# Performance work log

Measured on AMD Instinct MI355X. Metric: run time of the kernel, lower is better.

Reference implementation:

```python
import jax, jax.numpy as jnp
import numpy as np

N, D, H, F = 50000, 128, 8, 512
HD = D // H
EPS_BN = 1e-5


def _batchnorm(x, gamma, beta):
    # BatchNorm1d in training mode: per-feature batch stats over node dim
    m = x.mean(axis=0)
    v = x.var(axis=0)
    return (x - m) * jax.lax.rsqrt(v + EPS_BN) * gamma + beta


def setup_inputs() -> dict:
    key = jax.random.key(0)
    ks = jax.random.split(key, 12)
    s = 0.05
    return {
        "src": jax.random.normal(ks[0], (N, D), jnp.float32),
        "edge_index": jax.random.randint(ks[1], (2, 800000), 0, N, jnp.int64),
        "q_w": jax.random.normal(ks[2], (D, D), jnp.float32) * s,
        "q_b": jnp.zeros((D,), jnp.float32),
        "k_w": jax.random.normal(ks[3], (D, D), jnp.float32) * s,
        "v_w": jax.random.normal(ks[4], (D, D), jnp.float32) * s,
        "out_w": jax.random.normal(ks[5], (D, D), jnp.float32) * s,
        "out_b": jnp.zeros((D,), jnp.float32),
        "g1": jnp.ones((D,), jnp.float32),
        "b1": jnp.zeros((D,), jnp.float32),
        "lin1_w": jax.random.normal(ks[6], (F, D), jnp.float32) * s,
        "lin1_b": jnp.zeros((F,), jnp.float32),
        "lin2_w": jax.random.normal(ks[7], (D, F), jnp.float32) * s,
        "lin2_b": jnp.zeros((D,), jnp.float32),
        "g2": jnp.ones((D,), jnp.float32),
        "b2": jnp.zeros((D,), jnp.float32),
    }


def reference(src, edge_index, q_w, q_b, k_w, v_w, out_w, out_b,
              g1, b1, lin1_w, lin1_b, lin2_w, lin2_b, g2, b2):
    n = src.shape[0]
    # add self loops, then attention edge index is (dst=edge[1], src=edge[0])
    loops = jnp.arange(n, dtype=edge_index.dtype)
    ei = jnp.concatenate([edge_index, jnp.stack([loops, loops])], axis=1)
    e_src, e_dst = ei[0], ei[1]  # message flows e_src -> e_dst; query index = e_dst

    scaling = float(HD) ** (-0.5)
    q = ((src @ q_w.T + q_b) * scaling).reshape(n, H, HD)
    k = (src @ k_w.T).reshape(n, H, HD)
    v = (src @ v_w.T).reshape(n, H, HD)

    # per-edge scores [E, H]
    w = jnp.einsum("ehd,ehd->eh", q[e_dst], k[e_src])
    # deterministic segment softmax over edges grouped by destination node
    mx = jax.ops.segment_max(w, e_dst, num_segments=n)
    ex = jnp.exp(w - mx[e_dst])
    den = jax.ops.segment_sum(ex, e_dst, num_segments=n)
    attn_w = ex / (den[e_dst] + 1e-16)  # [E, H]

    # weighted scatter-add aggregation -> [n, H, HD]
    msgs = attn_w[:, :, None] * v[e_src]
    agg = jax.ops.segment_sum(msgs, e_dst, num_segments=n)

    attn_out = agg.reshape(n, D) @ out_w.T + out_b
    x = _batchnorm(src + attn_out, g1, b1)

    ff = jax.nn.leaky_relu(x @ lin1_w.T + lin1_b, negative_slope=0.01)
    ff = ff @ lin2_w.T + lin2_b
    x = _batchnorm(x + ff, g2, b2)
    return x
```

## Files before the change

### kernel.cpp

```cpp
#include <hip/hip_runtime.h>
#include <math.h>

#define D 128
#define H 8
#define HD 16

typedef __attribute__((ext_vector_type(8))) short bf16x8;
typedef __attribute__((ext_vector_type(4))) float f32x4;

__device__ __forceinline__ ushort f2bf(float x) {
    union { float f; unsigned u; } v; v.f = x;
    unsigned r = v.u + 0x7fffu + ((v.u >> 16) & 1u);
    return (ushort)(r >> 16);
}
__device__ __forceinline__ float bflo(unsigned u) {
    union { unsigned u; float f; } x; x.u = u << 16; return x.f;
}
__device__ __forceinline__ float bfhi(unsigned u) {
    union { unsigned u; float f; } x; x.u = u & 0xffff0000u; return x.f;
}
__device__ __forceinline__ float bf2f(short s) {
    union { unsigned u; float f; } x; x.u = ((unsigned)(ushort)s) << 16; return x.f;
}

__device__ __forceinline__ float dot16(const float* qf, uint4 a, uint4 b) {
    float w;
    w  = qf[0]  * bflo(a.x) + qf[1]  * bfhi(a.x);
    w += qf[2]  * bflo(a.y) + qf[3]  * bfhi(a.y);
    w += qf[4]  * bflo(a.z) + qf[5]  * bfhi(a.z);
    w += qf[6]  * bflo(a.w) + qf[7]  * bfhi(a.w);
    w += qf[8]  * bflo(b.x) + qf[9]  * bfhi(b.x);
    w += qf[10] * bflo(b.y) + qf[11] * bfhi(b.y);
    w += qf[12] * bflo(b.z) + qf[13] * bfhi(b.z);
    w += qf[14] * bflo(b.w) + qf[15] * bfhi(b.w);
    return w;
}
__device__ __forceinline__ void acc16(float* num, float e, uint4 a, uint4 b) {
    num[0]  = fmaf(e, bflo(a.x), num[0]);  num[1]  = fmaf(e, bfhi(a.x), num[1]);
    num[2]  = fmaf(e, bflo(a.y), num[2]);  num[3]  = fmaf(e, bfhi(a.y), num[3]);
    num[4]  = fmaf(e, bflo(a.z), num[4]);  num[5]  = fmaf(e, bfhi(a.z), num[5]);
    num[6]  = fmaf(e, bflo(a.w), num[6]);  num[7]  = fmaf(e, bfhi(a.w), num[7]);
    num[8]  = fmaf(e, bflo(b.x), num[8]);  num[9]  = fmaf(e, bfhi(b.x), num[9]);
    num[10] = fmaf(e, bflo(b.y), num[10]); num[11] = fmaf(e, bfhi(b.y), num[11]);
    num[12] = fmaf(e, bflo(b.z), num[12]); num[13] = fmaf(e, bfhi(b.z), num[13]);
    num[14] = fmaf(e, bflo(b.w), num[14]); num[15] = fmaf(e, bfhi(b.w), num[15]);
}

template<int AMODE, int EPI, int K, int MW>
__global__ __launch_bounds__(256)
void gemm_v2_kernel(const void* __restrict__ Ap,
                    const ushort* __restrict__ W,
                    const float* __restrict__ bias,
                    const void* __restrict__ extra,
                    const float* __restrict__ stats,
                    ushort* __restrict__ outb,
                    int N)
{
    constexpr int M   = MW * 4;
    constexpr int KC  = (K < 128) ? K : 128;
    constexpr int KT  = KC / 32;
    constexpr int NKC = K / KC;

    const int lane = threadIdx.x & 63, wave = threadIdx.x >> 6;
    const int lr = lane & 15, lq = lane >> 4;
    const int row0 = blockIdx.x * 32;
    const int c0w  = wave * MW;

    int ar0 = min(row0 + lr, N - 1);
    int ar1 = min(row0 + 16 + lr, N - 1);

    bf16x8 afr[2][KT];

    auto loadA = [&](int kc) {
        #pragma unroll
        for (int s = 0; s < 2; ++s) {
            int ar = s ? ar1 : ar0;
            if (AMODE == 0 || AMODE == 2) {
                const ushort* ap = (const ushort*)Ap + (size_t)ar * K + kc * KC + lq * 8;
                #pragma unroll
                for (int t = 0; t < KT; ++t) {
                    bf16x8 raw = *(const bf16x8*)(ap + t * 32);
                    if (AMODE == 0) {
                        afr[s][t] = raw;
                    } else {
                        int kb = kc * KC + t * 32 + lq * 8;
                        const float4* scp = (const float4*)(stats + 256 + kb);
                        const float4* shp = (const float4*)(stats + 384 + kb);
                        float4 sA = scp[0], sB = scp[1], hA = shp[0], hB = shp[1];
                        bf16x8 o;
                        o[0] = (short)f2bf(fmaf(bf2f(raw[0]), sA.x, hA.x));
                        o[1] = (short)f2bf(fmaf(bf2f(raw[1]), sA.y, hA.y));
                        o[2] = (short)f2bf(fmaf(bf2f(raw[2]), sA.z, hA.z));
                        o[3] = (short)f2bf(fmaf(bf2f(raw[3]), sA.w, hA.w));
                        o[4] = (short)f2bf(fmaf(bf2f(raw[4]), sB.x, hB.x));
                        o[5] = (short)f2bf(fmaf(bf2f(raw[5]), sB.y, hB.y));
                        o[6] = (short)f2bf(fmaf(bf2f(raw[6]), sB.z, hB.z));
                        o[7] = (short)f2bf(fmaf(bf2f(raw[7]), sB.w, hB.w));
                        afr[s][t] = o;
                    }
                }
            } else {
                const float* ap = (const float*)Ap + (size_t)ar * K + kc * KC + lq * 8;
                #pragma unroll
                for (int t = 0; t < KT; ++t) {
                    float4 f0 = *(const float4*)(ap + t * 32);
                    float4 f1 = *(const float4*)(ap + t * 32 + 4);
                    bf16x8 o;
                    o[0] = (short)f2bf(f0.x); o[1] = (short)f2bf(f0.y);
                    o[2] = (short)f2bf(f0.z); o[3] = (short)f2bf(f0.w);
                    o[4] = (short)f2bf(f1.x); o[5] = (short)f2bf(f1.y);
                    o[6] = (short)f2bf(f1.z); o[7] = (short)f2bf(f1.w);
                    afr[s][t] = o;
                }
            }
        }
    };

    if (NKC == 1) loadA(0);

    const float*  extf = (const float*)extra;
    const ushort* extb = (const ushort*)extra;

    #pragma unroll 1
    for (int cp = 0; cp < MW / 32; ++cp) {
        const int cbase = c0w + cp * 32;
        f32x4 acc[2][2] = {};

        #pragma unroll 1
        for (int kc = 0; kc < NKC; ++kc) {
            if (NKC > 1) loadA(kc);
            const ushort* wp0 = W + (size_t)(cbase + lr) * K + kc * KC + lq * 8;
            const ushort* wp1 = wp0 + (size_t)16 * K;
            #pragma unroll
            for (int t = 0; t < KT; ++t) {
                bf16x8 b0 = *(const bf16x8*)(wp0 + t * 32);
                bf16x8 b1 = *(const bf16x8*)(wp1 + t * 32);
                acc[0][0] = __builtin_amdgcn_mfma_f32_16x16x32_bf16(afr[0][t], b0, acc[0][0], 0, 0, 0);
                acc[1][0] = __builtin_amdgcn_mfma_f32_16x16x32_bf16(afr[1][t], b0, acc[1][0], 0, 0, 0);
                acc[0][1] = __builtin_amdgcn_mfma_f32_16x16x32_bf16(afr[0][t], b1, acc[0][1], 0, 0, 0);
                acc[1][1] = __builtin_amdgcn_mfma_f32_16x16x32_bf16(afr[1][t], b1, acc[1][1], 0, 0, 0);
            }
        }

        #pragma unroll
        for (int ct = 0; ct < 2; ++ct) {
            int col = cbase + ct * 16 + lr;
            float biasv = bias[col];
            float scv = 0.f, shv = 0.f;
            if (EPI == 4) { scv = stats[256 + col]; shv = stats[384 + col]; }
            #pragma unroll
            for (int s = 0; s < 2; ++s) {
                #pragma unroll
                for (int r = 0; r < 4; ++r) {
                    int grow = row0 + s * 16 + lq * 4 + r;
                    if (grow >= N) continue;
                    size_t o = (size_t)grow * M + col;
                    float v = acc[s][ct][r] + biasv;
                    if (EPI == 2) {
                        v = v > 0.f ? v : 0.01f * v;
                    } else if (EPI == 3) {
                        v += extf[o];
                    } else if (EPI == 4) {
                        v += fmaf(bf2f((short)extb[o]), scv, shv);
                    }
                    outb[o] = f2bf(v);
                }
            }
        }
    }
}

__global__ __launch_bounds__(256)
void convert_weights_kernel(const float* __restrict__ qw, const float* __restrict__ qb,
                            const float* __restrict__ kw, const float* __restrict__ vw,
                            const float* __restrict__ ow, const float* __restrict__ w1,
                            const float* __restrict__ w2,
                            ushort* __restrict__ wqkv, ushort* __restrict__ wout,
                            ushort* __restrict__ w1b, ushort* __restrict__ w2b,
                            float* __restrict__ bqkv)
{
    int i = blockIdx.x * 256 + threadIdx.x;
    if (i < 49152) {
        int row = i >> 7;
        float v;
        if (row < 128)      v = 0.25f * qw[i];
        else if (row < 256) v = kw[i - 16384];
        else                v = vw[i - 32768];
        wqkv[i] = f2bf(v);
        return;
    }
    int j = i - 49152;
    if (j < 16384) { wout[j] = f2bf(ow[j]); return; }
    j -= 16384;
    if (j < 65536) { w1b[j] = f2bf(w1[j]); return; }
    j -= 65536;
    if (j < 65536) { w2b[j] = f2bf(w2[j]); return; }
    j -= 65536;
    if (j < 384) bqkv[j] = (j < 128) ? 0.25f * qb[j] : 0.f;
}

__global__ __launch_bounds__(256)
void deg_count_kernel(const int* __restrict__ ei, long long E0, int* __restrict__ deg)
{
    long long e = (long long)blockIdx.x * 256 + threadIdx.x;
    if (e < E0) atomicAdd(&deg[ei[E0 + e]], 1);
}

__global__ __launch_bounds__(256)
void scan_block_sum(const int* __restrict__ deg, int n, int* __restrict__ bsum)
{
    __shared__ int sh[256];
    int i = blockIdx.x * 256 + threadIdx.x;
    sh[threadIdx.x] = (i < n) ? deg[i] : 0;
    __syncthreads();
    for (int ofs = 128; ofs > 0; ofs >>= 1) {
        if (threadIdx.x < ofs) sh[threadIdx.x] += sh[threadIdx.x + ofs];
        __syncthreads();
    }
    if (threadIdx.x == 0) bsum[blockIdx.x] = sh[0];
}

__global__ __launch_bounds__(256)
void scan_final(const int* __restrict__ deg, int n, const int* __restrict__ bsum,
                int nb, int* __restrict__ rowptr)
{
    __shared__ int sb[256];
    __shared__ int sh[256];
    int t = threadIdx.x;
    sb[t] = (t < nb) ? bsum[t] : 0;
    __syncthreads();
    for (int ofs = 1; ofs < 256; ofs <<= 1) {
        int v = (t >= ofs) ? sb[t - ofs] : 0;
        __syncthreads();
        sb[t] += v;
        __syncthreads();
    }
    int boff = (blockIdx.x == 0) ? 0 : sb[blockIdx.x - 1];

    int i = blockIdx.x * 256 + t;
    int v = (i < n) ? deg[i] : 0;
    sh[t] = v;
    __syncthreads();
    for (int ofs = 1; ofs < 256; ofs <<= 1) {
        int u = (t >= ofs) ? sh[t - ofs] : 0;
        __syncthreads();
        sh[t] += u;
        __syncthreads();
    }
    if (i < n) rowptr[i] = boff + sh[t] - v;
    if (i == n - 1) rowptr[n] = boff + sh[t];
}

__global__ __launch_bounds__(256)
void scatter_kernel(const int* __restrict__ ei, long long E0,
                    const int* __restrict__ rowptr, int* __restrict__ cnt,
                    int* __restrict__ col)
{
    long long e = (long long)blockIdx.x * 256 + threadIdx.x;
    if (e >= E0) return;
    int s = ei[e], d = ei[E0 + e];
    int pos = rowptr[d] + atomicAdd(&cnt[d], 1);
    col[pos] = s;
}

__global__ __launch_bounds__(256)
void gat_agg_kernel(const int* __restrict__ rowptr, const int* __restrict__ col,
                    const ushort* __restrict__ qkv, ushort* __restrict__ agg, int N)
{
    int node = blockIdx.x * 4 + (threadIdx.x >> 6);
    if (node >= N) return;
    int lane = threadIdx.x & 63;
    int es = lane >> 3, h = lane & 7;
    const uint4* Q = (const uint4*)qkv;

    const uint4* qp = Q + (size_t)node * 48 + h * 2;
    uint4 qa = qp[0], qb = qp[1];
    float qf[16];
    qf[0]=bflo(qa.x); qf[1]=bfhi(qa.x); qf[2]=bflo(qa.y); qf[3]=bfhi(qa.y);
    qf[4]=bflo(qa.z); qf[5]=bfhi(qa.z); qf[6]=bflo(qa.w); qf[7]=bfhi(qa.w);
    qf[8]=bflo(qb.x); qf[9]=bfhi(qb.x); qf[10]=bflo(qb.y); qf[11]=bfhi(qb.y);
    qf[12]=bflo(qb.z); qf[13]=bfhi(qb.z); qf[14]=bflo(qb.w); qf[15]=bfhi(qb.w);

    float num[16];
    #pragma unroll
    for (int i = 0; i < 16; i++) num[i] = 0.f;
    float den = 0.f;

    int beg = rowptr[node];
    int total = rowptr[node + 1] - beg + 1;
    for (int idx = es; idx < total; idx += 8) {
        int s = (idx == 0) ? node : col[beg + idx - 1];
        const uint4* rp = Q + (size_t)s * 48 + h * 2;
        uint4 ka = rp[16], kb = rp[17], va = rp[32], vb = rp[33];
        float ev = __expf(dot16(qf, ka, kb));
        den += ev;
        acc16(num, ev, va, vb);
    }

    #pragma unroll
    for (int m = 8; m < 64; m <<= 1) {
        den += __shfl_xor(den, m, 64);
        #pragma unroll
        for (int i = 0; i < 16; i++) num[i] += __shfl_xor(num[i], m, 64);
    }

    if (es == 0) {
        float inv = 1.f / (den + 1e-16f);
        uint4 o0, o1;
        o0.x = (uint)f2bf(num[0]*inv)  | ((uint)f2bf(num[1]*inv)  << 16);
        o0.y = (uint)f2bf(num[2]*inv)  | ((uint)f2bf(num[3]*inv)  << 16);
        o0.z = (uint)f2bf(num[4]*inv)  | ((uint)f2bf(num[5]*inv)  << 16);
        o0.w = (uint)f2bf(num[6]*inv)  | ((uint)f2bf(num[7]*inv)  << 16);
        o1.x = (uint)f2bf(num[8]*inv)  | ((uint)f2bf(num[9]*inv)  << 16);
        o1.y = (uint)f2bf(num[10]*inv) | ((uint)f2bf(num[11]*inv) << 16);
        o1.z = (uint)f2bf(num[12]*inv) | ((uint)f2bf(num[13]*inv) << 16);
        o1.w = (uint)f2bf(num[14]*inv) | ((uint)f2bf(num[15]*inv) << 16);
        uint4* op = (uint4*)(agg + (size_t)node * 128 + h * 16);
        op[0] = o0; op[1] = o1;
    }
}

__global__ __launch_bounds__(256)
void bn_stats_bf16_kernel(const ushort* __restrict__ y, int N, float* __restrict__ stats)
{
    int jp = threadIdx.x & 63;
    int q4 = threadIdx.x >> 6;
    int r = blockIdx.x * 256 + q4;
    int rend = min(N, (int)(blockIdx.x + 1) * 256);
    float s0 = 0.f, qq0 = 0.f, s1 = 0.f, qq1 = 0.f;
    const uint* yp = (const uint*)y;
    for (; r < rend; r += 4) {
        uint u = yp[(size_t)r * 64 + jp];
        float a = bflo(u), b = bfhi(u);
        s0 += a; qq0 += a * a; s1 += b; qq1 += b * b;
    }
    __shared__ float sh[4][64][4];
    sh[q4][jp][0] = s0; sh[q4][jp][1] = qq0; sh[q4][jp][2] = s1; sh[q4][jp][3] = qq1;
    __syncthreads();
    if (threadIdx.x < 128) {
        int p = threadIdx.x >> 1;
        int w = threadIdx.x & 1;
        float ss = 0.f, sq = 0.f;
        #pragma unroll
        for (int i = 0; i < 4; i++) { ss += sh[i][p][w * 2]; sq += sh[i][p][w * 2 + 1]; }
        unsafeAtomicAdd(&stats[2 * p + w], ss);
        unsafeAtomicAdd(&stats[128 + 2 * p + w], sq);
    }
}

__global__ void bn_finalize_kernel(float* __restrict__ stats,
                                   const float* __restrict__ g,
                                   const float* __restrict__ b, int N)
{
    int j = threadIdx.x;
    float mean = stats[j] / (float)N;
    float var  = stats[128 + j] / (float)N - mean * mean;
    float sc = g[j] * rsqrtf(var + 1e-5f);
    stats[256 + j] = sc;
    stats[384 + j] = b[j] - mean * sc;
}

__global__ __launch_bounds__(256)
void bn_apply_out_kernel(const ushort* __restrict__ y, const float* __restrict__ stats,
                         float* __restrict__ out, int total4)
{
    int i = blockIdx.x * 256 + threadIdx.x;
    if (i >= total4) return;
    uint2 u = reinterpret_cast<const uint2*>(y)[i];
    int j = (i * 4) & (D - 1);
    float4 v;
    v.x = bflo(u.x) * stats[256 + j + 0] + stats[384 + j + 0];
    v.y = bfhi(u.x) * stats[256 + j + 1] + stats[384 + j + 1];
    v.z = bflo(u.y) * stats[256 + j + 2] + stats[384 + j + 2];
    v.w = bfhi(u.y) * stats[256 + j + 3] + stats[384 + j + 3];
    reinterpret_cast<float4*>(out)[i] = v;
}

extern "C" void kernel_launch(void* const* d_in, const int* in_sizes, int n_in,
                              void* d_out, int out_size, void* d_ws, size_t ws_size,
                              hipStream_t stream)
{
    const float* src    = (const float*)d_in[0];
    const int*   ei     = (const int*)  d_in[1];
    const float* q_w    = (const float*)d_in[2];
    const float* q_b    = (const float*)d_in[3];
    const float* k_w    = (const float*)d_in[4];
    const float* v_w    = (const float*)d_in[5];
    const float* out_w  = (const float*)d_in[6];
    const float* out_b  = (const float*)d_in[7];
    const float* g1     = (const float*)d_in[8];
    const float* b1     = (const float*)d_in[9];
    const float* lin1_w = (const float*)d_in[10];
    const float* lin1_b = (const float*)d_in[11];
    const float* lin2_w = (const float*)d_in[12];
    const float* lin2_b = (const float*)d_in[13];
    const float* g2     = (const float*)d_in[14];
    const float* b2     = (const float*)d_in[15];

    const int N        = in_sizes[0] / D;
    const long long E0 = in_sizes[1] / 2;

    float* ws = (float*)d_ws;
    size_t off = 0;
    ushort* qkv  = (ushort*)(ws + off); off += (size_t)N * 192;
    ushort* agg  = (ushort*)(ws + off); off += (size_t)N * 64;
    ushort* y1b  = (ushort*)(ws + off); off += (size_t)N * 64;
    ushort* hid  = (ushort*)(ws + off); off += (size_t)N * 256;
    ushort* y2b  = (ushort*)(ws + off); off += (size_t)N * 64;
    ushort* wqkv = (ushort*)(ws + off); off += 24576;
    ushort* woutb= (ushort*)(ws + off); off += 8192;
    ushort* w1b  = (ushort*)(ws + off); off += 32768;
    ushort* w2b  = (ushort*)(ws + off); off += 32768;
    float*  bqkv = ws + off;            off += 384;
    size_t zero_start = off;
    int* deg    = (int*)(ws + off); off += N;
    int* cnt    = (int*)(ws + off); off += N;
    float* stats1 = ws + off; off += 512;
    float* stats2 = ws + off; off += 512;
    size_t zero_cnt = off - zero_start;
    int* rowptr = (int*)(ws + off); off += N + 1;
    int* bsum   = (int*)(ws + off); off += 256;
    int* col    = (int*)(ws + off); off += E0;

    hipMemsetAsync(ws + zero_start, 0, zero_cnt * sizeof(float), stream);

    dim3 blk(256);

    int cw_total = 49152 + 16384 + 65536 + 65536 + 384;
    hipLaunchKernelGGL(convert_weights_kernel, dim3((cw_total + 255) / 256), blk, 0, stream,
                       q_w, q_b, k_w, v_w, out_w, lin1_w, lin2_w,
                       wqkv, woutb, w1b, w2b, bqkv);

    dim3 gE0((unsigned)((E0 + 255) / 256));
    hipLaunchKernelGGL(deg_count_kernel, gE0, blk, 0, stream, ei, E0, deg);
    int nb = (N + 255) / 256;
    hipLaunchKernelGGL(scan_block_sum, dim3(nb), blk, 0, stream, deg, N, bsum);
    hipLaunchKernelGGL(scan_final, dim3(nb), blk, 0, stream, deg, N, bsum, nb, rowptr);
    hipLaunchKernelGGL(scatter_kernel, gE0, blk, 0, stream, ei, E0, rowptr, cnt, col);

    dim3 gG((N + 31) / 32);

    hipLaunchKernelGGL((gemm_v2_kernel<1, 0, 128, 96>), gG, blk, 0, stream,
                       src, wqkv, bqkv, nullptr, nullptr, qkv, N);

    hipLaunchKernelGGL(gat_agg_kernel, dim3((N + 3) / 4), blk, 0, stream,
                       rowptr, col, qkv, agg, N);

    hipLaunchKernelGGL((gemm_v2_kernel<0, 3, 128, 32>), gG, blk, 0, stream,
                       agg, woutb, out_b, src, nullptr, y1b, N);

    dim3 gS((N + 255) / 256);
    hipLaunchKernelGGL(bn_stats_bf16_kernel, gS, blk, 0, stream, y1b, N, stats1);
    hipLaunchKernelGGL(bn_finalize_kernel, dim3(1), dim3(128), 0, stream, stats1, g1, b1, N);

    hipLaunchKernelGGL((gemm_v2_kernel<2, 2, 128, 128>), gG, blk, 0, stream,
                       y1b, w1b, lin1_b, nullptr, stats1, hid, N);
    hipLaunchKernelGGL((gemm_v2_kernel<0, 4, 512, 32>), gG, blk, 0, stream,
                       hid, w2b, lin2_b, y1b, stats1, y2b, N);

    hipLaunchKernelGGL(bn_stats_bf16_kernel, gS, blk, 0, stream, y2b, N, stats2);
    hipLaunchKernelGGL(bn_finalize_kernel, dim3(1), dim3(128), 0, stream, stats2, g2, b2, N);
    int total4 = N * D / 4;
    hipLaunchKernelGGL(bn_apply_out_kernel, dim3((total4 + 255) / 256), blk, 0, stream,
                       y2b, stats2, (float*)d_out, total4);
}
```

Baseline: 470.0 us.

## Stage GEMM weights in swizzled LDS, split columns over grid, fuse small kernels

After: 475.9 us. No clear change (+1.3%).

```diff
diff --git a/kernel.cpp b/kernel.cpp
--- a/kernel.cpp
+++ b/kernel.cpp
@@ -46,61 +46,51 @@
     num[14] = fmaf(e, bflo(b.w), num[14]); num[15] = fmaf(e, bfhi(b.w), num[15]);
 }
 
-template<int AMODE, int EPI, int K, int MW>
-__global__ __launch_bounds__(256)
-void gemm_v2_kernel(const void* __restrict__ Ap,
+template<int AMODE, int EPI, int K, int M>
+__global__ __launch_bounds__(256)
+void gemm_v3_kernel(const void* __restrict__ Ap,
                     const ushort* __restrict__ W,
                     const float* __restrict__ bias,
                     const void* __restrict__ extra,
-                    const float* __restrict__ stats,
+                    const float* __restrict__ rawstats,
+                    const float* __restrict__ gg,
+                    const float* __restrict__ bb,
                     ushort* __restrict__ outb,
                     int N)
 {
-    constexpr int M   = MW * 4;
     constexpr int KC  = (K < 128) ? K : 128;
     constexpr int KT  = KC / 32;
     constexpr int NKC = K / KC;
 
-    const int lane = threadIdx.x & 63, wave = threadIdx.x >> 6;
+    __shared__ ushort Bs[128 * 128];
+    __shared__ float scs[128], shs[128];
+
+    const int tid = threadIdx.x;
+    const int lane = tid & 63, wave = tid >> 6;
     const int lr = lane & 15, lq = lane >> 4;
     const int row0 = blockIdx.x * 32;
-    const int c0w  = wave * MW;
+    const int colbase = blockIdx.y * 128;
 
     int ar0 = min(row0 + lr, N - 1);
     int ar1 = min(row0 + 16 + lr, N - 1);
 
+    if (AMODE == 2 && tid < 128) {
+        float mean = rawstats[tid] / (float)N;
+        float var  = rawstats[128 + tid] / (float)N - mean * mean;
+        float sc = gg[tid] * rsqrtf(var + 1e-5f);
+        scs[tid] = sc;
+        shs[tid] = bb[tid] - mean * sc;
+    }
+
     bf16x8 afr[2][KT];
-
-    auto loadA = [&](int kc) {
+    bf16x8 araw[2][KT];
+
+    auto loadAraw = [&](int kc) {
         #pragma unroll
         for (int s = 0; s < 2; ++s) {
             int ar = s ? ar1 : ar0;
-            if (AMODE == 0 || AMODE == 2) {
-                const ushort* ap = (const ushort*)Ap + (size_t)ar * K + kc * KC + lq * 8;
-                #pragma unroll
-                for (int t = 0; t < KT; ++t) {
-                    bf16x8 raw = *(const bf16x8*)(ap + t * 32);
-                    if (AMODE == 0) {
-                        afr[s][t] = raw;
-                    } else {
-                        int kb = kc * KC + t * 32 + lq * 8;
-                        const float4* scp = (const float4*)(stats + 256 + kb);
-                        const float4* shp = (const float4*)(stats + 384 + kb);
-                        float4 sA = scp[0], sB = scp[1], hA = shp[0], hB = shp[1];
-                        bf16x8 o;
-                        o[0] = (short)f2bf(fmaf(bf2f(raw[0]), sA.x, hA.x));
-                        o[1] = (short)f2bf(fmaf(bf2f(raw[1]), sA.y, hA.y));
-                        o[2] = (short)f2bf(fmaf(bf2f(raw[2]), sA.z, hA.z));
-                        o[3] = (short)f2bf(fmaf(bf2f(raw[3]), sA.w, hA.w));
-                        o[4] = (short)f2bf(fmaf(bf2f(raw[4]), sB.x, hB.x));
-                        o[5] = (short)f2bf(fmaf(bf2f(raw[5]), sB.y, hB.y));
-                        o[6] = (short)f2bf(fmaf(bf2f(raw[6]), sB.z, hB.z));
-                        o[7] = (short)f2bf(fmaf(bf2f(raw[7]), sB.w, hB.w));
-                        afr[s][t] = o;
-                    }
-                }
-            } else {
-                const float* ap = (const float*)Ap + (size_t)ar * K + kc * KC + lq * 8;
+            if (AMODE == 1) {
+                const float* ap = (const float*)Ap + (size_t)ar * K + lq * 8;
                 #pragma unroll
                 for (int t = 0; t < KT; ++t) {
                     float4 f0 = *(const float4*)(ap + t * 32);
@@ -112,76 +102,112 @@
                     o[6] = (short)f2bf(f1.z); o[7] = (short)f2bf(f1.w);
                     afr[s][t] = o;
                 }
+            } else {
+                const ushort* ap = (const ushort*)Ap + (size_t)ar * K + kc * KC + lq * 8;
+                #pragma unroll
+                for (int t = 0; t < KT; ++t) {
+                    bf16x8 raw = *(const bf16x8*)(ap + t * 32);
+                    if (AMODE == 0) afr[s][t] = raw;
+                    else            araw[s][t] = raw;
+                }
             }
         }
     };
 
-    if (NKC == 1) loadA(0);
+    auto stageB = [&](int kc) {
+        #pragma unroll
+        for (int it = 0; it < 8; ++it) {
+            int idx = tid + it * 256;
+            int c = idx >> 4, u = idx & 15;
+            const uint4* gp = (const uint4*)(W + (size_t)(colbase + c) * K + kc * KC) + u;
+            *(uint4*)&Bs[c * 128 + 8 * (u ^ (c & 7))] = *gp;
+        }
+    };
 
     const float*  extf = (const float*)extra;
     const ushort* extb = (const ushort*)extra;
 
+    f32x4 acc[2][2] = {};
+
     #pragma unroll 1
-    for (int cp = 0; cp < MW / 32; ++cp) {
-        const int cbase = c0w + cp * 32;
-        f32x4 acc[2][2] = {};
-
-        #pragma unroll 1
-        for (int kc = 0; kc < NKC; ++kc) {
-            if (NKC > 1) loadA(kc);
-            const ushort* wp0 = W + (size_t)(cbase + lr) * K + kc * KC + lq * 8;
-            const ushort* wp1 = wp0 + (size_t)16 * K;
+    for (int kc = 0; kc < NKC; ++kc) {
+        loadAraw(kc);
+        if (kc > 0) __syncthreads();
+        stageB(kc);
+        __syncthreads();
+
+        if (AMODE == 2) {
             #pragma unroll
-            for (int t = 0; t < KT; ++t) {
-                bf16x8 b0 = *(const bf16x8*)(wp0 + t * 32);
-                bf16x8 b1 = *(const bf16x8*)(wp1 + t * 32);
-                acc[0][0] = __builtin_amdgcn_mfma_f32_16x16x32_bf16(afr[0][t], b0, acc[0][0], 0, 0, 0);
-                acc[1][0] = __builtin_amdgcn_mfma_f32_16x16x32_bf16(afr[1][t], b0, acc[1][0], 0, 0, 0);
-                acc[0][1] = __builtin_amdgcn_mfma_f32_16x16x32_bf16(afr[0][t], b1, acc[0][1], 0, 0, 0);
-                acc[1][1] = __builtin_amdgcn_mfma_f32_16x16x32_bf16(afr[1][t], b1, acc[1][1], 0, 0, 0);
+            for (int s = 0; s < 2; ++s)
+                #pragma unroll
+                for (int t = 0; t < KT; ++t) {
+                    bf16x8 raw = araw[s][t];
+                    int kb = t * 32 + lq * 8;
+                    bf16x8 o;
+                    #pragma unroll
+                    for (int e = 0; e < 8; ++e)
+                        o[e] = (short)f2bf(fmaf(bf2f(raw[e]), scs[kb + e], shs[kb + e]));
+                    afr[s][t] = o;
+                }
+        }
+
+        const int cl0 = wave * 32 + lr;
+        const int cl1 = cl0 + 16;
+        #pragma unroll
+        for (int t = 0; t < KT; ++t) {
+            int u = t * 4 + lq;
+            bf16x8 b0 = *(const bf16x8*)&Bs[cl0 * 128 + 8 * (u ^ (cl0 & 7))];
+            bf16x8 b1 = *(const bf16x8*)&Bs[cl1 * 128 + 8 * (u ^ (cl1 & 7))];
+            acc[0][0] = __builtin_amdgcn_mfma_f32_16x16x32_bf16(afr[0][t], b0, acc[0][0], 0, 0, 0);
+            acc[1][0] = __builtin_amdgcn_mfma_f32_16x16x32_bf16(afr[1][t], b0, acc[1][0], 0, 0, 0);
+            acc[0][1] = __builtin_amdgcn_mfma_f32_16x16x32_bf16(afr[0][t], b1, acc[0][1], 0, 0, 0);
+            acc[1][1] = __builtin_amdgcn_mfma_f32_16x16x32_bf16(afr[1][t], b1, acc[1][1], 0, 0, 0);
+        }
+    }
+
+    #pragma unroll
+    for (int ct = 0; ct < 2; ++ct) {
+        int gcol = colbase + wave * 32 + ct * 16 + lr;
+        float biasv = bias[gcol];
+        float scv = 0.f, shv = 0.f;
+        if (EPI == 4) {
+            float mean = rawstats[gcol] / (float)N;
+            float var  = rawstats[128 + gcol] / (float)N - mean * mean;
+            scv = gg[gcol] * rsqrtf(var + 1e-5f);
+            shv = bb[gcol] - mean * scv;
+        }
+        #pragma unroll
+        for (int s = 0; s < 2; ++s) {
+            #pragma unroll
+            for (int r = 0; r < 4; ++r) {
+                int grow = row0 + s * 16 + lq * 4 + r;
+                if (grow >= N) continue;
+                size_t o = (size_t)grow * M + gcol;
+                float v = acc[s][ct][r] + biasv;
+                if (EPI == 2)      v = v > 0.f ? v : 0.01f * v;
+                else if (EPI == 3) v += extf[o];
+                else if (EPI == 4) v += fmaf(bf2f((short)extb[o]), scv, shv);
+                outb[o] = f2bf(v);
             }
         }
-
-        #pragma unroll
-        for (int ct = 0; ct < 2; ++ct) {
-            int col = cbase + ct * 16 + lr;
-            float biasv = bias[col];
-            float scv = 0.f, shv = 0.f;
-            if (EPI == 4) { scv = stats[256 + col]; shv = stats[384 + col]; }
-            #pragma unroll
-            for (int s = 0; s < 2; ++s) {
-                #pragma unroll
-                for (int r = 0; r < 4; ++r) {
-                    int grow = row0 + s * 16 + lq * 4 + r;
-                    if (grow >= N) continue;
-                    size_t o = (size_t)grow * M + col;
-                    float v = acc[s][ct][r] + biasv;
-                    if (EPI == 2) {
-                        v = v > 0.f ? v : 0.01f * v;
-                    } else if (EPI == 3) {
-                        v += extf[o];
-                    } else if (EPI == 4) {
-                        v += fmaf(bf2f((short)extb[o]), scv, shv);
-                    }
-                    outb[o] = f2bf(v);
-                }
-            }
-        }
-    }
-}
-
-__global__ __launch_bounds__(256)
-void convert_weights_kernel(const float* __restrict__ qw, const float* __restrict__ qb,
-                            const float* __restrict__ kw, const float* __restrict__ vw,
-                            const float* __restrict__ ow, const float* __restrict__ w1,
-                            const float* __restrict__ w2,
-                            ushort* __restrict__ wqkv, ushort* __restrict__ wout,
-                            ushort* __restrict__ w1b, ushort* __restrict__ w2b,
-                            float* __restrict__ bqkv)
-{
-    int i = blockIdx.x * 256 + threadIdx.x;
+    }
+}
+
+__global__ __launch_bounds__(256)
+void convert_deg_kernel(const float* __restrict__ qw, const float* __restrict__ qb,
+                        const float* __restrict__ kw, const float* __restrict__ vw,
+                        const float* __restrict__ ow, const float* __restrict__ w1,
+                        const float* __restrict__ w2,
+                        ushort* __restrict__ wqkv, ushort* __restrict__ wout,
+                        ushort* __restrict__ w1b, ushort* __restrict__ w2b,
+                        float* __restrict__ bqkv,
+                        const int* __restrict__ ei, long long E0,
+                        int* __restrict__ deg)
+{
+    long long i = (long long)blockIdx.x * 256 + threadIdx.x;
+    if (i < E0) atomicAdd(&deg[ei[E0 + i]], 1);
     if (i < 49152) {
-        int row = i >> 7;
+        int row = (int)i >> 7;
         float v;
         if (row < 128)      v = 0.25f * qw[i];
         else if (row < 256) v = kw[i - 16384];
@@ -189,7 +215,7 @@
         wqkv[i] = f2bf(v);
         return;
     }
-    int j = i - 49152;
+    long long j = i - 49152;
     if (j < 16384) { wout[j] = f2bf(ow[j]); return; }
     j -= 16384;
     if (j < 65536) { w1b[j] = f2bf(w1[j]); return; }
@@ -197,13 +223,6 @@
     if (j < 65536) { w2b[j] = f2bf(w2[j]); return; }
     j -= 65536;
     if (j < 384) bqkv[j] = (j < 128) ? 0.25f * qb[j] : 0.f;
-}
-
-__global__ __launch_bounds__(256)
-void deg_count_kernel(const int* __restrict__ ei, long long E0, int* __restrict__ deg)
-{
-    long long e = (long long)blockIdx.x * 256 + threadIdx.x;
-    if (e < E0) atomicAdd(&deg[ei[E0 + e]], 1);
 }
 
 __global__ __launch_bounds__(256)
@@ -348,31 +367,30 @@
     }
 }
 
-__global__ void bn_finalize_kernel(float* __restrict__ stats,
-                                   const float* __restrict__ g,
-                                   const float* __restrict__ b, int N)
-{
-    int j = threadIdx.x;
-    float mean = stats[j] / (float)N;
-    float var  = stats[128 + j] / (float)N - mean * mean;
-    float sc = g[j] * rsqrtf(var + 1e-5f);
-    stats[256 + j] = sc;
-    stats[384 + j] = b[j] - mean * sc;
-}
-
-__global__ __launch_bounds__(256)
-void bn_apply_out_kernel(const ushort* __restrict__ y, const float* __restrict__ stats,
-                         float* __restrict__ out, int total4)
-{
+__global__ __launch_bounds__(256)
+void bn_apply_out_kernel(const ushort* __restrict__ y, const float* __restrict__ rawstats,
+                         const float* __restrict__ g, const float* __restrict__ b,
+                         float* __restrict__ out, int total4, int N)
+{
+    __shared__ float scs[128], shs[128];
+    if (threadIdx.x < 128) {
+        int j = threadIdx.x;
+        float mean = rawstats[j] / (float)N;
+        float var  = rawstats[128 + j] / (float)N - mean * mean;
+        float sc = g[j] * rsqrtf(var + 1e-5f);
+        scs[j] = sc;
+        shs[j] = b[j] - mean * sc;
+    }
+    __syncthreads();
     int i = blockIdx.x * 256 + threadIdx.x;
     if (i >= total4) return;
     uint2 u = reinterpret_cast<const uint2*>(y)[i];
     int j = (i * 4) & (D - 1);
     float4 v;
-    v.x = bflo(u.x) * stats[256 + j + 0] + stats[384 + j + 0];
-    v.y = bfhi(u.x) * stats[256 + j + 1] + stats[384 + j + 1];
-    v.z = bflo(u.y) * stats[256 + j + 2] + stats[384 + j + 2];
-    v.w = bfhi(u.y) * stats[256 + j + 3] + stats[384 + j + 3];
+    v.x = bflo(u.x) * scs[j + 0] + shs[j + 0];
+    v.y = bfhi(u.x) * scs[j + 1] + shs[j + 1];
+    v.z = bflo(u.y) * scs[j + 2] + shs[j + 2];
+    v.w = bfhi(u.y) * scs[j + 3] + shs[j + 3];
     reinterpret_cast<float4*>(out)[i] = v;
 }
 
@@ -426,41 +444,38 @@
 
     dim3 blk(256);
 
-    int cw_total = 49152 + 16384 + 65536 + 65536 + 384;
-    hipLaunchKernelGGL(convert_weights_kernel, dim3((cw_total + 255) / 256), blk, 0, stream,
+    dim3 gE0((unsigned)((E0 + 255) / 256));
+    hipLaunchKernelGGL(convert_deg_kernel, gE0, blk, 0, stream,
                        q_w, q_b, k_w, v_w, out_w, lin1_w, lin2_w,
-                       wqkv, woutb, w1b, w2b, bqkv);
-
-    dim3 gE0((unsigned)((E0 + 255) / 256));
-    hipLaunchKernelGGL(deg_count_kernel, gE0, blk, 0, stream, ei, E0, deg);
+                       wqkv, woutb, w1b, w2b, bqkv, ei, E0, deg);
+
     int nb = (N + 255) / 256;
     hipLaunchKernelGGL(scan_block_sum, dim3(nb), blk, 0, stream, deg, N, bsum);
     hipLaunchKernelGGL(scan_final, dim3(nb), blk, 0, stream, deg, N, bsum, nb, rowptr);
     hipLaunchKernelGGL(scatter_kernel, gE0, blk, 0, stream, ei, E0, rowptr, cnt, col);
 
-    dim3 gG((N + 31) / 32);
-
-    hipLaunchKernelGGL((gemm_v2_kernel<1, 0, 128, 96>), gG, blk, 0, stream,
-                       src, wqkv, bqkv, nullptr, nullptr, qkv, N);
+    int gx = (N + 31) / 32;
+
+    hipLaunchKernelGGL((gemm_v3_kernel<1, 0, 128, 384>), dim3(gx, 3), blk, 0, stream,
+                       src, wqkv, bqkv, nullptr, nullptr, nullptr, nullptr, qkv, N);
 
     hipLaunchKernelGGL(gat_agg_kernel, dim3((N + 3) / 4), blk, 0, stream,
                        rowptr, col, qkv, agg, N);
 
-    hipLaunchKernelGGL((gemm_v2_kernel<0, 3, 128, 32>), gG, blk, 0, stream,
-                       agg, woutb, out_b, src, nullptr, y1b, N);
+    hipLaunchKernelGGL((gemm_v3_kernel<0, 3, 128, 128>), dim3(gx, 1), blk, 0, stream,
+                       agg, woutb, out_b, src, nullptr, nullptr, nullptr, y1b, N);
 
     dim3 gS((N + 255) / 256);
     hipLaunchKernelGGL(bn_stats_bf16_kernel, gS, blk, 0, stream, y1b, N, stats1);
-    hipLaunchKernelGGL(bn_finalize_kernel, dim3(1), dim3(128), 0, stream, stats1, g1, b1, N);
-
-    hipLaunchKernelGGL((gemm_v2_kernel<2, 2, 128, 128>), gG, blk, 0, stream,
-                       y1b, w1b, lin1_b, nullptr, stats1, hid, N);
-    hipLaunchKernelGGL((gemm_v2_kernel<0, 4, 512, 32>), gG, blk, 0, stream,
-                       hid, w2b, lin2_b, y1b, stats1, y2b, N);
+
+    hipLaunchKernelGGL((gemm_v3_kernel<2, 2, 128, 512>), dim3(gx, 4), blk, 0, stream,
+                       y1b, w1b, lin1_b, nullptr, stats1, g1, b1, hid, N);
+
+    hipLaunchKernelGGL((gemm_v3_kernel<0, 4, 512, 128>), dim3(gx, 1), blk, 0, stream,
+                       hid, w2b, lin2_b, y1b, stats1, g1, b1, y2b, N);
 
     hipLaunchKernelGGL(bn_stats_bf16_kernel, gS, blk, 0, stream, y2b, N, stats2);
-    hipLaunchKernelGGL(bn_finalize_kernel, dim3(1), dim3(128), 0, stream, stats2, g2, b2, N);
     int total4 = N * D / 4;
     hipLaunchKernelGGL(bn_apply_out_kernel, dim3((total4 + 255) / 256), blk, 0, stream,
-                       y2b, stats2, (float*)d_out, total4);
-}
+                       y2b, stats2, g2, b2, (float*)d_out, total4, N);
+}
```
